# Kernel optimization log

Hardware: AMD Instinct MI355X
Metric: run time of the kernel (lower is better)

The kernel has to match this reference:

```python
import jax, jax.numpy as jnp
import numpy as np

N, E, C, EMB, NB, L = 20000, 640000, 64, 32, 8, 2
MAX_RADIUS = 2.5
NUM_NEIGHBORS = 32.0
RH = 32  # radial MLP hidden


def setup_inputs() -> dict:
    key = jax.random.key(0)
    ks = jax.random.split(key, 24)
    g = lambda k, shape, fan: (jax.random.normal(k, shape, dtype=jnp.float32) / np.sqrt(fan).astype(np.float32))
    inp = {
        'x': jax.random.normal(ks[0], (N, 6), dtype=jnp.float32),
        'batch': jnp.zeros((N,), dtype=jnp.int64),
        'node_attr': jax.random.randint(ks[1], (N,), 0, 100),
        'edge_src': jax.random.randint(ks[2], (E,), 0, N),
        'edge_dst': jax.random.randint(ks[3], (E,), 0, N),
        'emb_table': jax.random.normal(ks[4], (100, EMB), dtype=jnp.float32),
        'uplift_M': jax.random.normal(ks[5], (C, 2), dtype=jnp.float32),
        'h': jnp.ones((L,), jnp.float32) * 0.01,
        'mix': jnp.ones((L,), jnp.float32) * 0.5,
        'rad_W1': g(ks[6], (L, NB, RH), NB),
        'rad_b1': jnp.zeros((L, RH), jnp.float32),
        'rad_W2': g(ks[7], (L, RH, 2 * C), RH),
        'lin1_s': g(ks[8], (L, C, C), C),
        'lin1_v': g(ks[9], (L, C, C), C),
        'lin2_s': g(ks[10], (L, C, 2 * C), C),
        'lin2_v': g(ks[11], (L, C, C), C),
        'sc_s_w': g(ks[12], (L, C, EMB, 2 * C), C * EMB),
        'sc_v_w': g(ks[13], (L, C, EMB, C), C * EMB),
        'si_s': g(ks[14], (L, C, C), C),
        'si_v': g(ks[15], (L, C, C), C),
    }
    return inp


def _forward(x, batch, node_attr, edge_src, edge_dst, emb_table, uplift_M, h, mix,
             rad_W1, rad_b1, rad_W2, lin1_s, lin1_v, lin2_s, lin2_v,
             sc_s_w, sc_v_w, si_s, si_v):
    n = x.shape[0]
    emb = emb_table[node_attr]                       # [N, EMB] node embedding
    # semi-unitarize uplift matrix: Q = M (M^T M)^{-1/2} == U V^T
    U, _, Vt = jnp.linalg.svd(uplift_M, full_matrices=False)
    Q = U @ Vt                                       # [C, 2]
    xv = x.reshape(n, 2, 3)
    y_s = jnp.zeros((n, C), x.dtype)                 # hidden scalars start at 0
    y_v = jnp.einsum('nkx,ck->ncx', xv, Q)           # uplift vectors [N,C,3]
    y = (y_s, y_v)
    y_old = y
    nbas = jnp.arange(1, NB + 1, dtype=x.dtype)
    inv_nn = 1.0 / np.sqrt(NUM_NEIGHBORS).astype(np.float32)
    for i in range(L):
        pos = x[:, :3]
        ev = pos[edge_src] - pos[edge_dst]           # [E,3]
        elen = jnp.linalg.norm(ev, axis=1)
        safe = jnp.maximum(elen, 1e-9)
        sh = np.float32(np.sqrt(3.0)) * ev / safe[:, None]   # 1x1o SH, component norm
        # bessel radial basis, scaled by sqrt(NB)
        ef = (np.float32(np.sqrt(2.0 / MAX_RADIUS)) *
              jnp.sin(nbas[None, :] * jnp.pi * safe[:, None] / MAX_RADIUS) / safe[:, None])
        ef = ef * np.float32(np.sqrt(NB))
        # smooth cutoff (e3nn tetris style)
        u = 2.0 * (elen / MAX_RADIUS - 1.0)
        cut = jnp.where(u > 0, 0.0, jnp.where(u < -2, 1.0, 0.5 * (1.0 - jnp.cos(jnp.pi * u))))
        ea = cut[:, None] * sh                       # [E,3] edge attr
        # linear pre-mix
        s1 = y[0] @ lin1_s[i]                        # [N,C]
        v1 = jnp.einsum('ncx,cd->ndx', y[1], lin1_v[i])  # [N,C,3]
        # radial MLP -> per-edge TP weights
        w = jax.nn.silu(ef @ rad_W1[i] + rad_b1[i]) @ rad_W2[i]  # [E,2C]
        w1, w2 = w[:, :C], w[:, C:]
        # tensor-product messages: 0e x 1o -> 1o ; 1o . 1o -> 0e
        msg_v = (w1 * s1[edge_src])[:, :, None] * ea[:, None, :]        # [E,C,3]
        msg_s = w2 * jnp.einsum('ecx,ex->ec', v1[edge_src], ea)         # [E,C]
        agg_s = jax.ops.segment_sum(msg_s, edge_dst, num_segments=n) * inv_nn
        agg_v = jax.ops.segment_sum(msg_v, edge_dst, num_segments=n) * inv_nn
        # post linear + node-attr self connection
        out_s = agg_s @ lin2_s[i] + jnp.einsum('nc,ne,ceo->no', y[0], emb, sc_s_w[i])   # [N,2C]
        out_v = (jnp.einsum('ncx,cd->ndx', agg_v, lin2_v[i]) +
                 jnp.einsum('ncx,ne,ceo->nox', y[1], emb, sc_v_w[i]))                   # [N,C,3]
        # gated nonlinearity
        g_s = jax.nn.silu(out_s[:, :C])
        g_v = jax.nn.sigmoid(out_s[:, C:])[:, :, None] * out_v
        # self interaction
        y2_s = y[0] @ si_s[i]
        y2_v = jnp.einsum('ncx,cd->ndx', y[1], si_v[i])
        # leapfrog update
        hh = h[i] * h[i]
        m = mix[i]
        new_s = 2.0 * y[0] - y_old[0] + hh * (m * g_s + (m - 1.0) * y2_s)
        new_v = 2.0 * y[1] - y_old[1] + hh * (m * g_v + (m - 1.0) * y2_v)
        y_old = y
        y = (new_s, new_v)
        x = jnp.einsum('ncx,ck->nkx', new_v, Q).reshape(n, 6)   # project
    return x


def reference(x, batch, node_attr, edge_src, edge_dst, emb_table, uplift_M, h, mix,
              rad_W1, rad_b1, rad_W2, lin1_s, lin1_v, lin2_s, lin2_v,
              sc_s_w, sc_v_w, si_s, si_v):
    return _forward(x, batch, node_attr, edge_src, edge_dst, emb_table, uplift_M, h, mix,
                    rad_W1, rad_b1, rad_W2, lin1_s, lin1_v, lin2_s, lin2_v,
                    sc_s_w, sc_v_w, si_s, si_v)
```

## Files before the change

kernel.cpp:

```cpp
#include <hip/hip_runtime.h>
#include <cstdio>
#include <cstdint>

#define CCH 64
#define EMBD 32
#define NBD 8
#define RHD 32
#define NATTR 100
#define TBINS 64

static constexpr float MAXR    = 2.5f;
static constexpr float INVNN   = 0.17677669529663687f;
static constexpr float EFK     = 2.5298221281347035f;
static constexpr float SQRT3   = 1.7320508075688772f;
static constexpr float PI_F    = 3.14159265358979323846f;

typedef __fp16 v2h __attribute__((ext_vector_type(2)));

__device__ __forceinline__ float sigm_(float x) { return 1.f / (1.f + __expf(-x)); }
__device__ __forceinline__ float silu_(float x) { return x / (1.f + __expf(-x)); }
__device__ __forceinline__ unsigned f2bfu(float f) {
    unsigned u = __float_as_uint(f);
    return (u + 0x7FFF + ((u >> 16) & 1)) >> 16;
}
__device__ __forceinline__ unsigned pack2(float lo, float hi) {
    return f2bfu(lo) | (f2bfu(hi) << 16);
}
__device__ __forceinline__ float ulo(unsigned u) { return __uint_as_float(u << 16); }
__device__ __forceinline__ float uhi(unsigned u) { return __uint_as_float(u & 0xFFFF0000u); }
__device__ __forceinline__ v2h u2h(unsigned u) { v2h h; __builtin_memcpy(&h, &u, 4); return h; }
__device__ __forceinline__ unsigned pkh(float a, float b) {
    v2h h = __builtin_amdgcn_cvt_pkrtz(a, b);
    unsigned u; __builtin_memcpy(&u, &h, 4); return u;
}
__device__ __forceinline__ unsigned short h1(float f) {
    __fp16 h = (__fp16)f; unsigned short s; __builtin_memcpy(&s, &h, 2); return s;
}
__device__ __forceinline__ float dot2(unsigned a, unsigned b, float c) {
    return __builtin_amdgcn_fdot2(u2h(a), u2h(b), c, false);
}
__device__ __forceinline__ float hlo(unsigned u) { v2h h = u2h(u); return (float)h.x; }
__device__ __forceinline__ float hhi(unsigned u) { v2h h = u2h(u); return (float)h.y; }

__global__ void kQ(const float* M, float* Q) {
    int c = threadIdx.x;
    float m0 = M[2*c], m1 = M[2*c+1];
    float a = m0*m0, b = m0*m1, d = m1*m1;
    for (int o = 32; o > 0; o >>= 1) {
        a += __shfl_xor(a, o); b += __shfl_xor(b, o); d += __shfl_xor(d, o);
    }
    float det = a*d - b*b;
    float s = sqrtf(det);
    float t = sqrtf(a + d + 2.f*s);
    float inv = 1.f / (s*t);
    float i00 = (d + s)*inv, i01 = -b*inv, i11 = (a + s)*inv;
    Q[2*c]   = m0*i00 + m1*i01;
    Q[2*c+1] = m0*i01 + m1*i11;
}

__global__ void kRadTab(const float* __restrict__ rW1, const float* __restrict__ rb1,
                        const float* __restrict__ rW2, unsigned* __restrict__ tab) {
    int bin = blockIdx.x;
    int l   = blockIdx.y;
    int lane = threadIdx.x;
    float r = bin * (MAXR / TBINS);
    float safe = fmaxf(r, 1e-9f);
    float invSafe = 1.f / safe;
    float th = PI_F * r * (1.f / MAXR);
    float s0, c0;
    __sincosf(th, &s0, &c0);
    __shared__ float hidS[RHD];
    if (lane < RHD) {
        float hs = rb1[l*RHD + lane];
        float sPrev = 0.f, sCur = s0, twoC = 2.f*c0;
        #pragma unroll
        for (int b = 0; b < NBD; ++b) {
            float efb = EFK * sCur * invSafe;
            hs = fmaf(efb, rW1[(l*NBD + b)*RHD + lane], hs);
            float sN = fmaf(twoC, sCur, -sPrev);
            sPrev = sCur; sCur = sN;
        }
        hidS[lane] = silu_(hs);
    }
    __syncthreads();
    float w1 = 0.f, w2 = 0.f;
    #pragma unroll
    for (int rr = 0; rr < RHD; ++rr) {
        float h = hidS[rr];
        w1 = fmaf(h, rW2[(l*RHD + rr)*128 + lane], w1);
        w2 = fmaf(h, rW2[(l*RHD + rr)*128 + 64 + lane], w2);
    }
    float cut = s0*s0;
    float coef = SQRT3 * cut * invSafe * INVNN;
    tab[((size_t)l*(TBINS+1) + bin)*64 + lane] = pack2(w1*coef, w2*coef);
}

__global__ void kPackW(const float* __restrict__ siv, unsigned* __restrict__ siVp) {
    int l = blockIdx.y;
    int i = blockIdx.x*256 + threadIdx.x;
    int cp = i >> 6, o = i & 63;
    siVp[l*2048 + i] = pkh(siv[l*4096 + (2*cp)*64 + o], siv[l*4096 + (2*cp+1)*64 + o]);
}

__global__ __launch_bounds__(256) void kInitLin(const float* __restrict__ x, const float* __restrict__ Qg,
        const float* __restrict__ L1v,
        float* __restrict__ yAv, float4* __restrict__ pos4,
        uint2* __restrict__ mv, int n) {
    __shared__ unsigned wPk[32*64];
    __shared__ __align__(16) unsigned bc[4][32][4];
    int t = threadIdx.x;
    for (int i = t; i < 32*64; i += 256) {
        int cp = i >> 6, o = i & 63;
        wPk[i] = pkh(L1v[(2*cp)*64 + o], L1v[(2*cp+1)*64 + o]);
    }
    __syncthreads();
    int lane = t & 63;
    int wid = t >> 6;
    float q0 = Qg[2*lane], q1 = Qg[2*lane+1];
    for (int node = blockIdx.x*4 + wid; node < n; node += gridDim.x*4) {
        const float* xr = x + (size_t)node*6;
        float x0 = xr[0], x1 = xr[1], x2 = xr[2], x3 = xr[3], x4 = xr[4], x5 = xr[5];
        float y0 = q0*x0 + q1*x3;
        float y1 = q0*x1 + q1*x4;
        float y2 = q0*x2 + q1*x5;
        float* yv = yAv + (size_t)node*192 + lane*3;
        yv[0] = y0; yv[1] = y1; yv[2] = y2;
        if (lane == 0) pos4[node] = (float4){x0, x1, x2, 0.f};
        {
            unsigned short* p = (unsigned short*)bc[wid][lane >> 1];
            int sub = lane & 1;
            p[0*2+sub] = h1(y0); p[1*2+sub] = h1(y1); p[2*2+sub] = h1(y2);
        }
        float a0 = 0.f, a1 = 0.f, a2 = 0.f;
        #pragma unroll 8
        for (int cp = 0; cp < 32; ++cp) {
            uint4 b = *(const uint4*)&bc[wid][cp][0];
            unsigned wp = wPk[cp*64 + lane];
            a0 = dot2(b.x, wp, a0);
            a1 = dot2(b.y, wp, a1);
            a2 = dot2(b.z, wp, a2);
        }
        mv[(size_t)node*64 + lane] = (uint2){ pack2(a0, a1), pack2(a2, 0.f) };
    }
}

__global__ void kHist(const int* dst, int* cnt, int e) {
    int i = blockIdx.x*blockDim.x + threadIdx.x;
    if (i < e) atomicAdd(&cnt[dst[i]], 1);
}

__global__ void kScan(const int* cnt, int* offs, int* curG0, int* curG1, int n) {
    __shared__ int part[1024];
    int t = threadIdx.x;
    int chunk = (n + 1023) >> 10;
    int lo = t*chunk, hi = min(lo + chunk, n);
    int s = 0;
    for (int i = lo; i < hi; ++i) s += cnt[i];
    part[t] = s;
    __syncthreads();
    for (int o = 1; o < 1024; o <<= 1) {
        int w = (t >= o) ? part[t - o] : 0;
        __syncthreads();
        part[t] += w;
        __syncthreads();
    }
    int run = part[t] - s;
    for (int i = lo; i < hi; ++i) {
        int cv = cnt[i];
        offs[i] = run; curG0[i] = run; curG1[i] = run;
        run += cv;
    }
    if (t == 1023) offs[n] = part[1023];
}

__global__ void kHistA(const int* __restrict__ attr, int* __restrict__ acnt, int n) {
    int i = blockIdx.x*256 + threadIdx.x;
    if (i < n) atomicAdd(&acnt[attr[i]], 1);
}
__global__ void kScanA(const int* __restrict__ acnt, int* __restrict__ acur) {
    __shared__ int part[128];
    int t = threadIdx.x;
    int v = (t < NATTR) ? acnt[t] : 0;
    part[t] = v;
    __syncthreads();
    for (int o = 1; o < 128; o <<= 1) {
        int w = (t >= o) ? part[t - o] : 0;
        __syncthreads();
        part[t] += w;
        __syncthreads();
    }
    if (t < NATTR) acur[t] = part[t] - v;
}
__global__ void kScatterA(const int* __restrict__ attr, int* __restrict__ acur,
                          int* __restrict__ nodeOrd, int n) {
    int i = blockIdx.x*256 + threadIdx.x;
    if (i < n) {
        int p = atomicAdd(&acur[attr[i]], 1);
        nodeOrd[p] = i;
    }
}

__global__ __launch_bounds__(256) void kGeom(const float4* __restrict__ pos4,
        const int* __restrict__ esrc, const int* __restrict__ edst,
        int* __restrict__ cur, uint4* __restrict__ rec, int e) {
    int i = blockIdx.x*256 + threadIdx.x;
    if (i >= e) return;
    int s = esrc[i], d = edst[i];
    float4 pa = pos4[s], pb = pos4[d];
    float ex = pa.x - pb.x, ey = pa.y - pb.y, ez = pa.z - pb.z;
    float el2 = ex*ex + ey*ey + ez*ez;
    if (el2 >= MAXR*MAXR) return;
    float elen = sqrtf(el2);
    float u = fminf(elen * ((float)TBINS / MAXR), 63.98f);
    int p = atomicAdd(&cur[d], 1);
    rec[p] = (uint4){ (unsigned)s, pkh(ex, ey), pkh(ez, u), 0u };
}

__global__ __launch_bounds__(256) void kT3(const float* __restrict__ embT,
        const float* __restrict__ scs, const float* __restrict__ scv,
        unsigned* __restrict__ TallU) {
    int cp = blockIdx.x, l = blockIdx.y, ag = blockIdx.z;
    int c0 = 2*cp, c1 = c0 + 1;
    __shared__ float sS0[32*128], sS1[32*128], sV0[32*64], sV1[32*64], sE[20*EMBD];
    int t = threadIdx.x;
    const float* p0 = scs + ((size_t)(l*CCH + c0)*EMBD)*128;
    const float* p1 = scs + ((size_t)(l*CCH + c1)*EMBD)*128;
    for (int i = t; i < 32*128; i += 256) { sS0[i] = p0[i]; sS1[i] = p1[i]; }
    const float* q0 = scv + ((size_t)(l*CCH + c0)*EMBD)*64;
    const float* q1 = scv + ((size_t)(l*CCH + c1)*EMBD)*64;
    for (int i = t; i < 32*64; i += 256) { sV0[i] = q0[i]; sV1[i] = q1[i]; }
    const float* eb = embT + (size_t)ag*20*EMBD;
    for (int i = t; i < 20*EMBD; i += 256) sE[i] = eb[i];
    __syncthreads();
    if (t < 128) {
        int o = t;
        for (int a = 0; a < 20; ++a) {
            float acc0 = 0.f, acc1 = 0.f;
            #pragma unroll
            for (int e = 0; e < EMBD; ++e) {
                float ev = sE[a*EMBD + e];
                acc0 = fmaf(ev, sS0[e*128 + o], acc0);
                acc1 = fmaf(ev, sS1[e*128 + o], acc1);
            }
            int aa = ag*20 + a;
            size_t idx = ((size_t)(l*NATTR + aa)*32 + cp)*64 + (o & 63);
            TallU[idx*4 + (o >> 6)] = pkh(acc0, acc1);
        }
    } else if (t < 192) {
        int o = t - 128;
        for (int a = 0; a < 20; ++a) {
            float acc0 = 0.f, acc1 = 0.f;
            #pragma unroll
            for (int e = 0; e < EMBD; ++e) {
                float ev = sE[a*EMBD + e];
                acc0 = fmaf(ev, sV0[e*64 + o], acc0);
                acc1 = fmaf(ev, sV1[e*64 + o], acc1);
            }
            int aa = ag*20 + a;
            size_t idx = ((size_t)(l*NATTR + aa)*32 + cp)*64 + o;
            TallU[idx*4 + 2] = pkh(acc0, acc1);
        }
    }
}

__global__ __launch_bounds__(256) void kLin1(const float* __restrict__ ys, const float* __restrict__ yv,
        const float* __restrict__ L1s, const float* __restrict__ L1v,
        uint2* __restrict__ mv, int n) {
    __shared__ uint2 wPk[32*64];
    __shared__ __align__(16) unsigned bc[4][32][4];
    int t = threadIdx.x;
    for (int i = t; i < 32*64; i += 256) {
        int cp = i >> 6, o = i & 63;
        wPk[i] = (uint2){ pkh(L1s[(2*cp)*64 + o], L1s[(2*cp+1)*64 + o]),
                          pkh(L1v[(2*cp)*64 + o], L1v[(2*cp+1)*64 + o]) };
    }
    __syncthreads();
    int lane = t & 63;
    int wid = t >> 6;
    for (int node = blockIdx.x*4 + wid; node < n; node += gridDim.x*4) {
        float ys_r = ys[(size_t)node*64 + lane];
        const float* yvp = yv + (size_t)node*192 + lane*3;
        float y0 = yvp[0], y1 = yvp[1], y2 = yvp[2];
        {
            unsigned short* p = (unsigned short*)bc[wid][lane >> 1];
            int sub = lane & 1;
            p[0*2+sub] = h1(y0); p[1*2+sub] = h1(y1);
            p[2*2+sub] = h1(y2); p[3*2+sub] = h1(ys_r);
        }
        float as = 0.f, a0 = 0.f, a1 = 0.f, a2 = 0.f;
        #pragma unroll 8
        for (int cp = 0; cp < 32; ++cp) {
            uint4 b = *(const uint4*)&bc[wid][cp][0];
            uint2 wp = wPk[cp*64 + lane];
            as = dot2(b.w, wp.x, as);
            a0 = dot2(b.x, wp.y, a0);
            a1 = dot2(b.y, wp.y, a1);
            a2 = dot2(b.z, wp.y, a2);
        }
        mv[(size_t)node*64 + lane] = (uint2){ pack2(a0, a1), pack2(a2, as) };
    }
}

template<int WITHV>
__global__ __launch_bounds__(256) void kAgg(const uint4* __restrict__ rec,
        const uint2* __restrict__ mv,
        const int* __restrict__ offs, const int* __restrict__ endA,
        const unsigned* __restrict__ tabG,
        float* __restrict__ aggS, float* __restrict__ aggV, int n) {
    __shared__ unsigned tab[(TBINS+1)*64];
    __shared__ float red[4][64][4];
    int t = threadIdx.x;
    for (int i = t; i < (TBINS+1)*64; i += 256) tab[i] = tabG[i];
    __syncthreads();
    int lane = t & 63;
    int wid = t >> 6;

    for (int node = blockIdx.x; node < n; node += gridDim.x) {
        int beg = offs[node], end = endA[node];
        float accS = 0.f, av0 = 0.f, av1 = 0.f, av2 = 0.f;
        int idx = beg + wid;
        uint4 r0 = (uint4){0u,0u,0u,0u}, r1 = r0;
        uint2 m0 = (uint2){0u,0u}, m1 = m0;
        if (idx < end)     { r0 = rec[idx];   m0 = mv[(size_t)r0.x*64 + lane]; }
        if (idx + 4 < end) { r1 = rec[idx+4]; m1 = mv[(size_t)r1.x*64 + lane]; }
        for (; idx < end; idx += 4) {
            uint4 r2 = (uint4){0u,0u,0u,0u};
            uint2 m2 = (uint2){0u,0u};
            if (idx + 8 < end) { r2 = rec[idx+8]; m2 = mv[(size_t)r2.x*64 + lane]; }
            float ex = hlo(r0.y), ey = hhi(r0.y);
            float ez = hlo(r0.z), u = hhi(r0.z);
            int i0 = (int)u;
            float fr = u - (float)i0;
            unsigned t0 = tab[i0*64 + lane];
            unsigned t1 = tab[i0*64 + 64 + lane];
            float w1 = fmaf(fr, ulo(t1) - ulo(t0), ulo(t0));
            float w2 = fmaf(fr, uhi(t1) - uhi(t0), uhi(t0));
            float dv = ulo(m0.x)*ex + uhi(m0.x)*ey + ulo(m0.y)*ez;
            accS = fmaf(w2, dv, accS);
            if (WITHV) {
                float tt = w1 * uhi(m0.y);
                av0 = fmaf(tt, ex, av0); av1 = fmaf(tt, ey, av1); av2 = fmaf(tt, ez, av2);
            }
            r0 = r1; m0 = m1; r1 = r2; m1 = m2;
        }
        red[wid][lane][0] = accS; red[wid][lane][1] = av0;
        red[wid][lane][2] = av1;  red[wid][lane][3] = av2;
        __syncthreads();
        if (wid == 0) {
            float rs = red[0][lane][0] + red[1][lane][0] + red[2][lane][0] + red[3][lane][0];
            aggS[(size_t)node*64 + lane] = rs;
            float r0s = red[0][lane][1] + red[1][lane][1] + red[2][lane][1] + red[3][lane][1];
            float r1s = red[0][lane][2] + red[1][lane][2] + red[2][lane][2] + red[3][lane][2];
            float r2s = red[0][lane][3] + red[1][lane][3] + red[2][lane][3] + red[3][lane][3];
            float* ap = aggV + (size_t)node*192 + lane*3;
            ap[0] = r0s; ap[1] = r1s; ap[2] = r2s;
        }
        __syncthreads();
    }
}

template<int L0>
__global__ __launch_bounds__(256) void kOutComb(const float* __restrict__ ys, const float* __restrict__ yv,
        const float* __restrict__ yoldv,
        const float* __restrict__ aggS, const float* __restrict__ aggV,
        const int* __restrict__ attr, const int* __restrict__ nodeOrd,
        const float* __restrict__ L2s, const float* __restrict__ L2v,
        const uint4* __restrict__ Tall,
        const float* __restrict__ siS, const unsigned* __restrict__ siVp, const float* __restrict__ Qg,
        const float* __restrict__ hArr, const float* __restrict__ mArr, int li,
        float* __restrict__ newS, float* __restrict__ newV,
        float4* __restrict__ pos4out, float* __restrict__ xout6, int n) {
    __shared__ uint4 wAll[32*64];
    __shared__ __align__(16) unsigned bc[4][32][8];
    int t = threadIdx.x;
    for (int i = t; i < 32*64; i += 256) {
        int cp = i >> 6, o = i & 63;
        wAll[i] = (uint4){ pkh(L2s[(2*cp)*128 + o],      L2s[(2*cp+1)*128 + o]),
                           pkh(L2s[(2*cp)*128 + 64 + o], L2s[(2*cp+1)*128 + 64 + o]),
                           pkh(L2v[(2*cp)*64 + o], L2v[(2*cp+1)*64 + o]),
                           L0 ? 0u : pkh(siS[(2*cp)*64 + o], siS[(2*cp+1)*64 + o]) };
    }
    __syncthreads();
    int lane = t & 63;
    int wid = t >> 6;
    unsigned svr[32];
    #pragma unroll
    for (int cp = 0; cp < 32; ++cp) svr[cp] = siVp[cp*64 + lane];
    float hh = hArr[li]; hh *= hh;
    float m = mArr[li];
    float q0 = Qg[2*lane], q1 = Qg[2*lane+1];
    int nw = gridDim.x*4;
    int chunk = (n + nw - 1) / nw;
    int start = (blockIdx.x*4 + wid) * chunk;
    int stop = min(start + chunk, n);
    for (int ii = start; ii < stop; ++ii) {
        int node = nodeOrd[ii];
        int a = attr[node];
        const unsigned* tA = (const unsigned*)(Tall + (size_t)a*2048);
        float as_r = aggS[(size_t)node*64 + lane];
        float ys_r = L0 ? 0.f : ys[(size_t)node*64 + lane];
        const float* avp = aggV + (size_t)node*192 + lane*3;
        float av0 = avp[0], av1 = avp[1], av2 = avp[2];
        const float* yvp = yv + (size_t)node*192 + lane*3;
        float by0 = yvp[0], by1 = yvp[1], by2 = yvp[2];
        {
            unsigned short* p = (unsigned short*)bc[wid][lane >> 1];
            int sub = lane & 1;
            p[0*2+sub] = h1(as_r); p[1*2+sub] = L0 ? (unsigned short)0 : h1(ys_r);
            p[2*2+sub] = h1(av0);  p[3*2+sub] = h1(by0);
            p[4*2+sub] = h1(av1);  p[5*2+sub] = h1(by1);
            p[6*2+sub] = h1(av2);  p[7*2+sub] = h1(by2);
        }
        float oS0=0.f, oS1=0.f, ov0=0.f, ov1=0.f, ov2=0.f;
        float q2s=0.f, qv0=0.f, qv1=0.f, qv2=0.f;
        #pragma unroll 4
        for (int cp = 0; cp < 32; ++cp) {
            uint4 bA = *(const uint4*)&bc[wid][cp][0];
            uint4 bB = *(const uint4*)&bc[wid][cp][4];
            uint4 wv4 = wAll[cp*64 + lane];
            if (L0) {
                unsigned tv = tA[(cp*64 + lane)*4 + 2];
                oS0 = dot2(bA.x, wv4.x, oS0);
                oS1 = dot2(bA.x, wv4.y, oS1);
                ov0 = dot2(bA.z, wv4.z, dot2(bA.w, tv, ov0));
                ov1 = dot2(bB.x, wv4.z, dot2(bB.y, tv, ov1));
                ov2 = dot2(bB.z, wv4.z, dot2(bB.w, tv, ov2));
            } else {
                uint4 tw = ((const uint4*)tA)[cp*64 + lane];
                oS0 = dot2(bA.x, wv4.x, dot2(bA.y, tw.x, oS0));
                oS1 = dot2(bA.x, wv4.y, dot2(bA.y, tw.y, oS1));
                ov0 = dot2(bA.z, wv4.z, dot2(bA.w, tw.z, ov0));
                ov1 = dot2(bB.x, wv4.z, dot2(bB.y, tw.z, ov1));
                ov2 = dot2(bB.z, wv4.z, dot2(bB.w, tw.z, ov2));
                q2s = dot2(bA.y, wv4.w, q2s);
            }
            qv0 = dot2(bA.w, svr[cp], qv0);
            qv1 = dot2(bB.y, svr[cp], qv1);
            qv2 = dot2(bB.w, svr[cp], qv2);
        }
        float gs = silu_(oS0);
        float sg = sigm_(oS1);
        float gv0 = sg*ov0, gv1 = sg*ov1, gv2 = sg*ov2;
        float ns, nv0, nv1, nv2;
        if (L0) {
            ns  = hh*m*gs;
            nv0 = by0 + hh*(m*gv0 + (m-1.f)*qv0);
            nv1 = by1 + hh*(m*gv1 + (m-1.f)*qv1);
            nv2 = by2 + hh*(m*gv2 + (m-1.f)*qv2);
        } else {
            const float* yop = yoldv + (size_t)node*192 + lane*3;
            ns  = 2.f*ys_r + hh*(m*gs + (m-1.f)*q2s);
            nv0 = 2.f*by0 - yop[0] + hh*(m*gv0 + (m-1.f)*qv0);
            nv1 = 2.f*by1 - yop[1] + hh*(m*gv1 + (m-1.f)*qv1);
            nv2 = 2.f*by2 - yop[2] + hh*(m*gv2 + (m-1.f)*qv2);
        }
        if (L0) {
            newS[(size_t)node*64 + lane] = ns;
            float* np = newV + (size_t)node*192 + lane*3;
            np[0] = nv0; np[1] = nv1; np[2] = nv2;
        }
        float p00 = nv0*q0, p01 = nv1*q0, p02 = nv2*q0;
        float p10 = nv0*q1, p11 = nv1*q1, p12 = nv2*q1;
        for (int o = 32; o > 0; o >>= 1) {
            p00 += __shfl_xor(p00, o); p01 += __shfl_xor(p01, o); p02 += __shfl_xor(p02, o);
            p10 += __shfl_xor(p10, o); p11 += __shfl_xor(p11, o); p12 += __shfl_xor(p12, o);
        }
        if (lane == 0) {
            if (L0) {
                pos4out[node] = (float4){p00, p01, p02, 0.f};
            } else {
                float* xp = xout6 + (size_t)node*6;
                xp[0] = p00; xp[1] = p01; xp[2] = p02;
                xp[3] = p10; xp[4] = p11; xp[5] = p12;
            }
        }
    }
}

extern "C" void kernel_launch(void* const* d_in, const int* in_sizes, int n_in,
                              void* d_out, int out_size, void* d_ws, size_t ws_size,
                              hipStream_t stream) {
    const float* x        = (const float*)d_in[0];
    const int*   nattr    = (const int*)  d_in[2];
    const int*   esrc     = (const int*)  d_in[3];
    const int*   edst     = (const int*)  d_in[4];
    const float* embT     = (const float*)d_in[5];
    const float* upM      = (const float*)d_in[6];
    const float* hArr     = (const float*)d_in[7];
    const float* mArr     = (const float*)d_in[8];
    const float* rW1      = (const float*)d_in[9];
    const float* rb1      = (const float*)d_in[10];
    const float* rW2      = (const float*)d_in[11];
    const float* l1s      = (const float*)d_in[12];
    const float* l1v      = (const float*)d_in[13];
    const float* l2s      = (const float*)d_in[14];
    const float* l2v      = (const float*)d_in[15];
    const float* scs      = (const float*)d_in[16];
    const float* scv      = (const float*)d_in[17];
    const float* sis      = (const float*)d_in[18];
    const float* siv      = (const float*)d_in[19];
    int n = in_sizes[0] / 6;
    int e = in_sizes[3];
    float* out = (float*)d_out;

    float* w = (float*)d_ws;
    float* Q    = w; w += 128;
    float* yAv  = w; w += (size_t)n*192;
    float* yBs  = w; w += (size_t)n*64;
    float* yBv  = w; w += (size_t)n*192;
    float* aggS = w; w += (size_t)n*64;
    float* aggV = w; w += (size_t)n*192;
    float4* pos4 = (float4*)w; w += (size_t)n*4;
    uint2* mv    = (uint2*)w;  w += (size_t)n*128;
    uint4* Tall  = (uint4*)w;  w += (size_t)2*NATTR*2048*4;
    unsigned* radTab = (unsigned*)w; w += (size_t)2*(TBINS+1)*64;
    unsigned* siVp = (unsigned*)w; w += (size_t)2*2048;
    uint4* rec = (uint4*)w; w += (size_t)e*4;
    int* cnt   = (int*)w;
    int* offs  = cnt + n;
    int* curG0 = offs + (n + 1);
    int* curG1 = curG0 + n;
    int* acnt  = curG1 + n;
    int* acur  = acnt + NATTR;
    int* nodeOrd = acur + NATTR;
    size_t need = (size_t)((char*)(nodeOrd + n) - (char*)d_ws);
    if (need > ws_size) {
        fprintf(stderr, "kernel_launch: ws too small (%zu > %zu)\n", need, ws_size);
        return;
    }

    const int AGG_GRID  = 1792;
    const int OC_GRID   = 1024;
    const int LIN_GRID  = 2048;
    int eb = (e + 255)/256;
    int nb = (n + 255)/256;

    kQ<<<1, 64, 0, stream>>>(upM, Q);
    hipMemsetAsync(cnt, 0, (size_t)n*sizeof(int), stream);
    hipMemsetAsync(acnt, 0, (size_t)NATTR*sizeof(int), stream);
    kHist<<<eb, 256, 0, stream>>>(edst, cnt, e);
    kScan<<<1, 1024, 0, stream>>>(cnt, offs, curG0, curG1, n);
    kHistA<<<nb, 256, 0, stream>>>(nattr, acnt, n);
    kScanA<<<1, 128, 0, stream>>>(acnt, acur);
    kScatterA<<<nb, 256, 0, stream>>>(nattr, acur, nodeOrd, n);
    kT3<<<dim3(32, 2, 5), 256, 0, stream>>>(embT, scs, scv, (unsigned*)Tall);
    kRadTab<<<dim3(TBINS+1, 2), 64, 0, stream>>>(rW1, rb1, rW2, radTab);
    kPackW<<<dim3(8, 2), 256, 0, stream>>>(siv, siVp);
    kInitLin<<<LIN_GRID, 256, 0, stream>>>(x, Q, l1v, yAv, pos4, mv, n);

    kGeom<<<eb, 256, 0, stream>>>(pos4, esrc, edst, curG0, rec, e);
    kAgg<0><<<AGG_GRID, 256, 0, stream>>>(rec, mv, offs, curG0, radTab, aggS, aggV, n);
    kOutComb<1><<<OC_GRID, 256, 0, stream>>>(nullptr, yAv, nullptr, aggS, aggV, nattr, nodeOrd,
                                  l2s, l2v, Tall, sis, siVp, Q, hArr, mArr, 0,
                                  yBs, yBv, pos4, out, n);
    kLin1<<<LIN_GRID, 256, 0, stream>>>(yBs, yBv, l1s + 4096, l1v + 4096, mv, n);
    kGeom<<<eb, 256, 0, stream>>>(pos4, esrc, edst, curG1, rec, e);
    kAgg<1><<<AGG_GRID, 256, 0, stream>>>(rec, mv, offs, curG1,
                                  radTab + (size_t)(TBINS+1)*64, aggS, aggV, n);
    kOutComb<0><<<OC_GRID, 256, 0, stream>>>(yBs, yBv, yAv, aggS, aggV, nattr, nodeOrd,
                                  l2s + (size_t)64*128, l2v + (size_t)64*64,
                                  Tall + (size_t)NATTR*2048,
                                  sis + 4096, siVp + 2048, Q, hArr, mArr, 1,
                                  nullptr, nullptr, nullptr, out, n);
}
```

Baseline: 571.5 us.

## Assign output-combine blocks per node attribute and stage its weight table in LDS

Output-combine blocks are now mapped to node-attribute groups, KBLK blocks per attribute, using per-attribute offsets from the attribute scan. Each block loads its attribute's self-connection table into shared memory once instead of fetching it from global memory per node. The inner channel loop is also fully unrolled. The trade-offs are higher LDS use (32KB extra for layer 1), which can reduce occupancy, and load imbalance because attribute group sizes vary (about 200 nodes each over 5 blocks).

```diff
diff --git a/kernel.cpp b/kernel.cpp
--- a/kernel.cpp
+++ b/kernel.cpp
@@ -8,6 +8,7 @@
 #define RHD 32
 #define NATTR 100
 #define TBINS 64
+#define KBLK 5
 
 static constexpr float MAXR    = 2.5f;
 static constexpr float INVNN   = 0.17677669529663687f;
@@ -177,7 +178,7 @@
     int i = blockIdx.x*256 + threadIdx.x;
     if (i < n) atomicAdd(&acnt[attr[i]], 1);
 }
-__global__ void kScanA(const int* __restrict__ acnt, int* __restrict__ acur) {
+__global__ void kScanA(const int* __restrict__ acnt, int* __restrict__ aoffs, int* __restrict__ acur) {
     __shared__ int part[128];
     int t = threadIdx.x;
     int v = (t < NATTR) ? acnt[t] : 0;
@@ -189,7 +190,7 @@
         part[t] += w;
         __syncthreads();
     }
-    if (t < NATTR) acur[t] = part[t] - v;
+    if (t < NATTR) { aoffs[t] = part[t] - v; acur[t] = part[t] - v; }
 }
 __global__ void kScatterA(const int* __restrict__ attr, int* __restrict__ acur,
                           int* __restrict__ nodeOrd, int n) {
@@ -363,7 +364,7 @@
 __global__ __launch_bounds__(256) void kOutComb(const float* __restrict__ ys, const float* __restrict__ yv,
         const float* __restrict__ yoldv,
         const float* __restrict__ aggS, const float* __restrict__ aggV,
-        const int* __restrict__ attr, const int* __restrict__ nodeOrd,
+        const int* __restrict__ nodeOrd, const int* __restrict__ aoffs, const int* __restrict__ acnt,
         const float* __restrict__ L2s, const float* __restrict__ L2v,
         const uint4* __restrict__ Tall,
         const float* __restrict__ siS, const unsigned* __restrict__ siVp, const float* __restrict__ Qg,
@@ -371,8 +372,13 @@
         float* __restrict__ newS, float* __restrict__ newV,
         float4* __restrict__ pos4out, float* __restrict__ xout6, int n) {
     __shared__ uint4 wAll[32*64];
+    __shared__ uint4 tallB[L0 ? 1 : 2048];
+    __shared__ unsigned tallS[L0 ? 2048 : 1];
     __shared__ __align__(16) unsigned bc[4][32][8];
     int t = threadIdx.x;
+    int a   = blockIdx.x / KBLK;
+    int sub = blockIdx.x % KBLK;
+    const unsigned* tAU = (const unsigned*)(Tall + (size_t)a*2048);
     for (int i = t; i < 32*64; i += 256) {
         int cp = i >> 6, o = i & 63;
         wAll[i] = (uint4){ pkh(L2s[(2*cp)*128 + o],      L2s[(2*cp+1)*128 + o]),
@@ -380,6 +386,8 @@
                            pkh(L2v[(2*cp)*64 + o], L2v[(2*cp+1)*64 + o]),
                            L0 ? 0u : pkh(siS[(2*cp)*64 + o], siS[(2*cp+1)*64 + o]) };
     }
+    if (L0) { for (int i = t; i < 2048; i += 256) tallS[i] = tAU[i*4 + 2]; }
+    else    { for (int i = t; i < 2048; i += 256) tallB[i] = ((const uint4*)tAU)[i]; }
     __syncthreads();
     int lane = t & 63;
     int wid = t >> 6;
@@ -389,14 +397,9 @@
     float hh = hArr[li]; hh *= hh;
     float m = mArr[li];
     float q0 = Qg[2*lane], q1 = Qg[2*lane+1];
-    int nw = gridDim.x*4;
-    int chunk = (n + nw - 1) / nw;
-    int start = (blockIdx.x*4 + wid) * chunk;
-    int stop = min(start + chunk, n);
-    for (int ii = start; ii < stop; ++ii) {
+    int beg = aoffs[a], endb = beg + acnt[a];
+    for (int ii = beg + sub*4 + wid; ii < endb; ii += KBLK*4) {
         int node = nodeOrd[ii];
-        int a = attr[node];
-        const unsigned* tA = (const unsigned*)(Tall + (size_t)a*2048);
         float as_r = aggS[(size_t)node*64 + lane];
         float ys_r = L0 ? 0.f : ys[(size_t)node*64 + lane];
         const float* avp = aggV + (size_t)node*192 + lane*3;
@@ -405,28 +408,28 @@
         float by0 = yvp[0], by1 = yvp[1], by2 = yvp[2];
         {
             unsigned short* p = (unsigned short*)bc[wid][lane >> 1];
-            int sub = lane & 1;
-            p[0*2+sub] = h1(as_r); p[1*2+sub] = L0 ? (unsigned short)0 : h1(ys_r);
-            p[2*2+sub] = h1(av0);  p[3*2+sub] = h1(by0);
-            p[4*2+sub] = h1(av1);  p[5*2+sub] = h1(by1);
-            p[6*2+sub] = h1(av2);  p[7*2+sub] = h1(by2);
+            int sub2 = lane & 1;
+            p[0*2+sub2] = h1(as_r); p[1*2+sub2] = L0 ? (unsigned short)0 : h1(ys_r);
+            p[2*2+sub2] = h1(av0);  p[3*2+sub2] = h1(by0);
+            p[4*2+sub2] = h1(av1);  p[5*2+sub2] = h1(by1);
+            p[6*2+sub2] = h1(av2);  p[7*2+sub2] = h1(by2);
         }
         float oS0=0.f, oS1=0.f, ov0=0.f, ov1=0.f, ov2=0.f;
         float q2s=0.f, qv0=0.f, qv1=0.f, qv2=0.f;
-        #pragma unroll 4
+        #pragma unroll
         for (int cp = 0; cp < 32; ++cp) {
             uint4 bA = *(const uint4*)&bc[wid][cp][0];
             uint4 bB = *(const uint4*)&bc[wid][cp][4];
             uint4 wv4 = wAll[cp*64 + lane];
             if (L0) {
-                unsigned tv = tA[(cp*64 + lane)*4 + 2];
+                unsigned tv = tallS[cp*64 + lane];
                 oS0 = dot2(bA.x, wv4.x, oS0);
                 oS1 = dot2(bA.x, wv4.y, oS1);
                 ov0 = dot2(bA.z, wv4.z, dot2(bA.w, tv, ov0));
                 ov1 = dot2(bB.x, wv4.z, dot2(bB.y, tv, ov1));
                 ov2 = dot2(bB.z, wv4.z, dot2(bB.w, tv, ov2));
             } else {
-                uint4 tw = ((const uint4*)tA)[cp*64 + lane];
+                uint4 tw = tallB[cp*64 + lane];
                 oS0 = dot2(bA.x, wv4.x, dot2(bA.y, tw.x, oS0));
                 oS1 = dot2(bA.x, wv4.y, dot2(bA.y, tw.y, oS1));
                 ov0 = dot2(bA.z, wv4.z, dot2(bA.w, tw.z, ov0));
@@ -521,7 +524,8 @@
     int* curG0 = offs + (n + 1);
     int* curG1 = curG0 + n;
     int* acnt  = curG1 + n;
-    int* acur  = acnt + NATTR;
+    int* aoffs = acnt + NATTR;
+    int* acur  = aoffs + NATTR;
     int* nodeOrd = acur + NATTR;
     size_t need = (size_t)((char*)(nodeOrd + n) - (char*)d_ws);
     if (need > ws_size) {
@@ -530,7 +534,7 @@
     }
 
     const int AGG_GRID  = 1792;
-    const int OC_GRID   = 1024;
+    const int OC_GRID   = NATTR*KBLK;
     const int LIN_GRID  = 2048;
     int eb = (e + 255)/256;
     int nb = (n + 255)/256;
@@ -541,7 +545,7 @@
     kHist<<<eb, 256, 0, stream>>>(edst, cnt, e);
     kScan<<<1, 1024, 0, stream>>>(cnt, offs, curG0, curG1, n);
     kHistA<<<nb, 256, 0, stream>>>(nattr, acnt, n);
-    kScanA<<<1, 128, 0, stream>>>(acnt, acur);
+    kScanA<<<1, 128, 0, stream>>>(acnt, aoffs, acur);
     kScatterA<<<nb, 256, 0, stream>>>(nattr, acur, nodeOrd, n);
     kT3<<<dim3(32, 2, 5), 256, 0, stream>>>(embT, scs, scv, (unsigned*)Tall);
     kRadTab<<<dim3(TBINS+1, 2), 64, 0, stream>>>(rW1, rb1, rW2, radTab);
@@ -550,14 +554,16 @@
 
     kGeom<<<eb, 256, 0, stream>>>(pos4, esrc, edst, curG0, rec, e);
     kAgg<0><<<AGG_GRID, 256, 0, stream>>>(rec, mv, offs, curG0, radTab, aggS, aggV, n);
-    kOutComb<1><<<OC_GRID, 256, 0, stream>>>(nullptr, yAv, nullptr, aggS, aggV, nattr, nodeOrd,
+    kOutComb<1><<<OC_GRID, 256, 0, stream>>>(nullptr, yAv, nullptr, aggS, aggV,
+                                  nodeOrd, aoffs, acnt,
                                   l2s, l2v, Tall, sis, siVp, Q, hArr, mArr, 0,
                                   yBs, yBv, pos4, out, n);
     kLin1<<<LIN_GRID, 256, 0, stream>>>(yBs, yBv, l1s + 4096, l1v + 4096, mv, n);
     kGeom<<<eb, 256, 0, stream>>>(pos4, esrc, edst, curG1, rec, e);
     kAgg<1><<<AGG_GRID, 256, 0, stream>>>(rec, mv, offs, curG1,
                                   radTab + (size_t)(TBINS+1)*64, aggS, aggV, n);
-    kOutComb<0><<<OC_GRID, 256, 0, stream>>>(yBs, yBv, yAv, aggS, aggV, nattr, nodeOrd,
+    kOutComb<0><<<OC_GRID, 256, 0, stream>>>(yBs, yBv, yAv, aggS, aggV,
+                                  nodeOrd, aoffs, acnt,
                                   l2s + (size_t)64*128, l2v + (size_t)64*64,
                                   Tall + (size_t)NATTR*2048,
                                   sis + 4096, siVp + 2048, Q, hArr, mArr, 1,
```

After: 551.6 us. 3.5% less time.
